# Performance work log

Hardware: AMD Instinct MI355X
Metric: run time of the kernel (lower is better)

## Reference

```python
import jax, jax.numpy as jnp
import numpy as np

# Dimensions (production-scale molecular density evaluation)
S = 5        # n_species (element types)
NR = 3       # n_radial functions per element (max_funs)
NA = 3       # max_angular_moment -> l in {1,2,3}
F = NR * NA  # total terms (k=1)
B, M, N = 8, 4096, 64  # batch molecules, grid points, atoms
EPS = 1e-12


def setup_inputs() -> dict:
    key = jax.random.key(0)
    k1, k2, k3, k4, k5, k6 = jax.random.split(key, 6)
    dv = jax.random.normal(k1, (B, M, N, 3), jnp.float32)           # displacement grid_point - atom
    coefficients = jax.random.normal(k2, (B, N, F, 3), jnp.float32)  # per-atom anisotropic coeff vectors
    labels = jax.random.randint(k3, (B, N), 0, S)                    # species index per atom
    a = jax.random.uniform(k4, (S, NR), jnp.float32, 0.5, 2.0)       # amplitudes
    b = jax.random.uniform(k5, (S, NR), jnp.float32, 0.5, 3.0)       # exponents
    p = jax.random.uniform(k6, (S, NR), jnp.float32, 0.0, 2.0)       # radial powers
    return {"dv": dv, "coefficients": coefficients, "labels": labels, "a": a, "b": b, "p": p}


def _legendre(x, l):
    # Legendre polynomial P_l(x) for l in {1,2,3}; l broadcasts over the term dim
    p1 = x
    p2 = 0.5 * (3.0 * x * x - 1.0)
    p3 = 0.5 * (5.0 * x * x * x - 3.0 * x)
    return jnp.where(l == 1, p1, jnp.where(l == 2, p2, p3))


def reference(dv, coefficients, labels, a, b, p):
    # expand radial params across the angular terms (repeat_interleave along dim 1): [S, F]
    a_e = jnp.repeat(a, NA, axis=1)
    b_e = jnp.repeat(b, NA, axis=1)
    p_e = jnp.repeat(p, NA, axis=1)
    # per-atom label gather (expand_parameter): [B, N, F]
    a_g = a_e[labels]
    b_g = b_e[labels]
    p_g = p_e[labels]
    # distances: [B, M, N]
    r = jnp.linalg.norm(dv, axis=-1)
    r4 = r[..., None]                                   # [B, M, N, 1]
    # generalized exponential kernel a * r^p * exp(-b r): [B, M, N, F]
    kern = a_g[:, None] * r4 ** p_g[:, None] * jnp.exp(-b_g[:, None] * r4)
    # anisotropic angular part: |c| * P_l(cos angle(dv, c))
    cnorm = jnp.linalg.norm(coefficients, axis=-1)      # [B, N, F]
    cunit = coefficients / jnp.maximum(cnorm[..., None], EPS)
    cos = jnp.einsum('bmnd,bnfd->bmnf', dv, cunit) / jnp.maximum(r4, EPS)
    l_arr = (jnp.arange(F) % NA) + 1                    # 1,2,3 cycling (qi pattern)
    q = _legendre(cos, l_arr)                           # [B, M, N, F]
    dens = kern * cnorm[:, None] * q                    # [B, M, N, F]
    # accumulate over terms, then over atoms (density += k; density.sum(2))
    return dens.sum(axis=(2, 3))                        # [B, M]
```

## Files before the change

### kernel.cpp

```cpp
#include <hip/hip_runtime.h>

#define Bb  8
#define Mm  4096
#define Nn  64
#define Ff  9
#define Ss  5
#define NRr 3

constexpr int REC = 48;
constexpr int MT  = 32;
constexpr int STR = 195;

__global__ __launch_bounds__(256, 4)
void HarmonicGenAMD_25786983645325_kernel(
    const float* __restrict__ dv,
    const float* __restrict__ coef,
    const int*   __restrict__ labels,
    const float* __restrict__ pa,
    const float* __restrict__ pb,
    const float* __restrict__ pp,
    float*       __restrict__ out)
{
    __shared__ __align__(16) float dvs[MT * STR];
    __shared__ __align__(16) float tabs[Nn * REC];
    __shared__ float red[128];

    const int tid = threadIdx.x;
    const int blk = blockIdx.x;
    const int b   = blk >> 7;
    const int m0  = (blk & 127) * MT;

    const float* g = dv + ((size_t)b * Mm + m0) * (Nn * 3);
#pragma unroll
    for (int it = 0; it < 6; ++it) {
        const int i   = it * 1024 + tid * 4;
        const int row = i / 192;
        const int col = i - row * 192;
        const float4 v = *(const float4*)(g + row * 192 + col);
        float* d = &dvs[row * STR + col];
        d[0] = v.x; d[1] = v.y; d[2] = v.z; d[3] = v.w;
    }

    if (tid < Nn) {
        const int s = labels[b * Nn + tid];
        float4 h0, h1;
        h0.x = pb[s * NRr + 0] * 1.44269504088896340736f;  h0.y = pp[s * NRr + 0];
        h0.z = pb[s * NRr + 1] * 1.44269504088896340736f;  h0.w = pp[s * NRr + 1];
        h1.x = pb[s * NRr + 2] * 1.44269504088896340736f;  h1.y = pp[s * NRr + 2];
        h1.z = 0.0f; h1.w = 0.0f;
        *(float4*)(&tabs[tid * REC + 0]) = h0;
        *(float4*)(&tabs[tid * REC + 4]) = h1;
    }
    for (int i = tid; i < Nn * Ff; i += 256) {
        const int n = i / Ff;
        const int f = i - n * Ff;
        const int j = f / 3;
        const int s = labels[b * Nn + n];
        const float* c = coef + ((size_t)(b * Nn + n) * Ff + f) * 3;
        const float cx = c[0], cy = c[1], cz = c[2];
        const float cn  = sqrtf(cx * cx + cy * cy + cz * cz);
        const float inv = 1.0f / fmaxf(cn, 1e-12f);
        float4 q;
        q.x = pa[s * NRr + j] * cn;
        q.y = cx * inv; q.z = cy * inv; q.w = cz * inv;
        *(float4*)(&tabs[n * REC + 8 + f * 4]) = q;
    }
    __syncthreads();

    const int lane = tid & 63;
    const int w    = tid >> 6;
    const int m    = lane & 31;
    const int h    = lane >> 5;
    const float* drow = &dvs[m * STR];

    float acc = 0.0f;
#pragma unroll 2
    for (int t = 0; t < 8; ++t) {
        const int n = w * 16 + t * 2 + h;
        const float* rec = &tabs[n * REC];
        const float x = drow[n * 3 + 0];
        const float y = drow[n * 3 + 1];
        const float z = drow[n * 3 + 2];
        const float r2   = __fmaf_rn(x, x, __fmaf_rn(y, y, z * z));
        const float rinv = __builtin_amdgcn_rsqf(r2);
        const float r    = r2 * rinv;
        const float l2r  = 0.5f * __builtin_amdgcn_logf(r2);
        const float dnx = x * rinv, dny = y * rinv, dnz = z * rinv;

        const float4 h0 = *(const float4*)(rec);
        const float2 h1 = *(const float2*)(rec + 4);
        float ek[3];
        ek[0] = __builtin_amdgcn_exp2f(__fmaf_rn(h0.y, l2r, -h0.x * r));
        ek[1] = __builtin_amdgcn_exp2f(__fmaf_rn(h0.w, l2r, -h0.z * r));
        ek[2] = __builtin_amdgcn_exp2f(__fmaf_rn(h1.y, l2r, -h1.x * r));
#pragma unroll
        for (int f = 0; f < Ff; ++f) {
            const float4 e = *(const float4*)(rec + 8 + f * 4);
            const float c = __fmaf_rn(dnx, e.y, __fmaf_rn(dny, e.z, dnz * e.w));
            float q;
            if      (f % 3 == 0) q = c;
            else if (f % 3 == 1) q = __fmaf_rn(1.5f * c, c, -0.5f);
            else                 q = c * __fmaf_rn(2.5f * c, c, -1.5f);
            acc = __fmaf_rn(e.x * ek[f / 3], q, acc);
        }
    }

    acc += __shfl_down(acc, 32, 64);
    if (h == 0) red[w * MT + m] = acc;
    __syncthreads();
    if (tid < MT) {
        out[(size_t)b * Mm + m0 + tid] =
            red[tid] + red[MT + tid] + red[2 * MT + tid] + red[3 * MT + tid];
    }
}

extern "C" void kernel_launch(void* const* d_in, const int* in_sizes, int n_in,
                              void* d_out, int out_size, void* d_ws, size_t ws_size,
                              hipStream_t stream) {
    const float* dv   = (const float*)d_in[0];
    const float* coef = (const float*)d_in[1];
    const int*   lab  = (const int*)d_in[2];
    const float* pa   = (const float*)d_in[3];
    const float* pb   = (const float*)d_in[4];
    const float* pp   = (const float*)d_in[5];
    float* out = (float*)d_out;

    dim3 grid(Bb * (Mm / MT));
    HarmonicGenAMD_25786983645325_kernel<<<grid, 256, 0, stream>>>(
        dv, coef, lab, pa, pb, pp, out);
}
```

Before: 84.78 us.

## Process two grid points per thread to reuse per-atom table loads

Doubles the grid-point tile per block to 64, so each thread evaluates two grid points against the same atom record. The coefficient and parameter LDS loads are then shared across two evaluations. The grid is halved and the per-block LDS for dv doubles, which lowers the occupancy hint to 2 blocks per CU. Register pressure also rises.

Result: no change. 84.83 us (+0.1%).

```diff
diff --git a/kernel.cpp b/kernel.cpp
--- a/kernel.cpp
+++ b/kernel.cpp
@@ -8,10 +8,10 @@
 #define NRr 3
 
 constexpr int REC = 48;
-constexpr int MT  = 32;
+constexpr int MT  = 64;
 constexpr int STR = 195;
 
-__global__ __launch_bounds__(256, 4)
+__global__ __launch_bounds__(256, 2)
 void HarmonicGenAMD_25786983645325_kernel(
     const float* __restrict__ dv,
     const float* __restrict__ coef,
@@ -23,16 +23,16 @@
 {
     __shared__ __align__(16) float dvs[MT * STR];
     __shared__ __align__(16) float tabs[Nn * REC];
-    __shared__ float red[128];
+    __shared__ float red[256];
 
     const int tid = threadIdx.x;
     const int blk = blockIdx.x;
-    const int b   = blk >> 7;
-    const int m0  = (blk & 127) * MT;
+    const int b   = blk >> 6;
+    const int m0  = (blk & 63) * MT;
 
     const float* g = dv + ((size_t)b * Mm + m0) * (Nn * 3);
 #pragma unroll
-    for (int it = 0; it < 6; ++it) {
+    for (int it = 0; it < 12; ++it) {
         const int i   = it * 1024 + tid * 4;
         const int row = i / 192;
         const int col = i - row * 192;
@@ -69,48 +69,66 @@
 
     const int lane = tid & 63;
     const int w    = tid >> 6;
-    const int m    = lane & 31;
+    const int mb   = lane & 31;
     const int h    = lane >> 5;
-    const float* drow = &dvs[m * STR];
+    const float* dlo = &dvs[mb * STR];
+    const float* dhi = &dvs[(mb + 32) * STR];
 
-    float acc = 0.0f;
+    float acc0 = 0.0f, acc1 = 0.0f;
 #pragma unroll 2
     for (int t = 0; t < 8; ++t) {
         const int n = w * 16 + t * 2 + h;
         const float* rec = &tabs[n * REC];
-        const float x = drow[n * 3 + 0];
-        const float y = drow[n * 3 + 1];
-        const float z = drow[n * 3 + 2];
-        const float r2   = __fmaf_rn(x, x, __fmaf_rn(y, y, z * z));
-        const float rinv = __builtin_amdgcn_rsqf(r2);
-        const float r    = r2 * rinv;
-        const float l2r  = 0.5f * __builtin_amdgcn_logf(r2);
-        const float dnx = x * rinv, dny = y * rinv, dnz = z * rinv;
+        const float x0 = dlo[n * 3 + 0], y0 = dlo[n * 3 + 1], z0 = dlo[n * 3 + 2];
+        const float x1 = dhi[n * 3 + 0], y1 = dhi[n * 3 + 1], z1 = dhi[n * 3 + 2];
+
+        const float r2a  = __fmaf_rn(x0, x0, __fmaf_rn(y0, y0, z0 * z0));
+        const float r2b  = __fmaf_rn(x1, x1, __fmaf_rn(y1, y1, z1 * z1));
+        const float ria  = __builtin_amdgcn_rsqf(r2a);
+        const float rib  = __builtin_amdgcn_rsqf(r2b);
+        const float ra   = r2a * ria;
+        const float rb   = r2b * rib;
+        const float la   = 0.5f * __builtin_amdgcn_logf(r2a);
+        const float lb   = 0.5f * __builtin_amdgcn_logf(r2b);
+        const float ax = x0 * ria, ay = y0 * ria, az = z0 * ria;
+        const float bx = x1 * rib, by = y1 * rib, bz = z1 * rib;
 
         const float4 h0 = *(const float4*)(rec);
         const float2 h1 = *(const float2*)(rec + 4);
-        float ek[3];
-        ek[0] = __builtin_amdgcn_exp2f(__fmaf_rn(h0.y, l2r, -h0.x * r));
-        ek[1] = __builtin_amdgcn_exp2f(__fmaf_rn(h0.w, l2r, -h0.z * r));
-        ek[2] = __builtin_amdgcn_exp2f(__fmaf_rn(h1.y, l2r, -h1.x * r));
+        float eka[3], ekb[3];
+        eka[0] = __builtin_amdgcn_exp2f(__fmaf_rn(h0.y, la, -h0.x * ra));
+        ekb[0] = __builtin_amdgcn_exp2f(__fmaf_rn(h0.y, lb, -h0.x * rb));
+        eka[1] = __builtin_amdgcn_exp2f(__fmaf_rn(h0.w, la, -h0.z * ra));
+        ekb[1] = __builtin_amdgcn_exp2f(__fmaf_rn(h0.w, lb, -h0.z * rb));
+        eka[2] = __builtin_amdgcn_exp2f(__fmaf_rn(h1.y, la, -h1.x * ra));
+        ekb[2] = __builtin_amdgcn_exp2f(__fmaf_rn(h1.y, lb, -h1.x * rb));
 #pragma unroll
         for (int f = 0; f < Ff; ++f) {
             const float4 e = *(const float4*)(rec + 8 + f * 4);
-            const float c = __fmaf_rn(dnx, e.y, __fmaf_rn(dny, e.z, dnz * e.w));
-            float q;
-            if      (f % 3 == 0) q = c;
-            else if (f % 3 == 1) q = __fmaf_rn(1.5f * c, c, -0.5f);
-            else                 q = c * __fmaf_rn(2.5f * c, c, -1.5f);
-            acc = __fmaf_rn(e.x * ek[f / 3], q, acc);
+            const float ca = __fmaf_rn(ax, e.y, __fmaf_rn(ay, e.z, az * e.w));
+            const float cb = __fmaf_rn(bx, e.y, __fmaf_rn(by, e.z, bz * e.w));
+            float qa, qb;
+            if (f % 3 == 0)      { qa = ca;                               qb = cb; }
+            else if (f % 3 == 1) { qa = __fmaf_rn(1.5f * ca, ca, -0.5f);  qb = __fmaf_rn(1.5f * cb, cb, -0.5f); }
+            else                 { qa = ca * __fmaf_rn(2.5f * ca, ca, -1.5f);
+                                   qb = cb * __fmaf_rn(2.5f * cb, cb, -1.5f); }
+            const float Aek_a = e.x * eka[f / 3];
+            const float Aek_b = e.x * ekb[f / 3];
+            acc0 = __fmaf_rn(Aek_a, qa, acc0);
+            acc1 = __fmaf_rn(Aek_b, qb, acc1);
         }
     }
 
-    acc += __shfl_down(acc, 32, 64);
-    if (h == 0) red[w * MT + m] = acc;
+    acc0 += __shfl_down(acc0, 32, 64);
+    acc1 += __shfl_down(acc1, 32, 64);
+    if (h == 0) {
+        red[w * 64 + mb]      = acc0;
+        red[w * 64 + 32 + mb] = acc1;
+    }
     __syncthreads();
     if (tid < MT) {
         out[(size_t)b * Mm + m0 + tid] =
-            red[tid] + red[MT + tid] + red[2 * MT + tid] + red[3 * MT + tid];
+            red[tid] + red[64 + tid] + red[128 + tid] + red[192 + tid];
     }
 }
 
```
